# Performance work log

Hardware: AMD Instinct MI355X
Metric: run time of the kernel (lower is better)

The kernel has to match this reference:

```python
import jax, jax.numpy as jnp
import numpy as np

GROUPS = 64; SIDE = 8; STEPS = 8
TAU = 1.0; FLOOR = 1e-4; EPS = 1e-4
MU = 1.0; DT = 0.1; GAMMA = 0.1
FLOW_W = 1.0; LOCAL_W = 0.5; KEEP_RATIO = 0.5


def _with_floor(m):
    n = m.shape[-1]
    mask = 1.0 - jnp.eye(n, dtype=m.dtype)
    return jnp.maximum(m * mask, FLOOR * mask)


def _norm_scores(s):
    mean = s.mean(axis=1, keepdims=True)
    std = jnp.clip(s.std(axis=1, ddof=1, keepdims=True), 1e-6, None)  # torch unbiased std
    return (s - mean) / std


def _router_core(tokens, cls_token, W, grid_h, grid_w):
    B, P, D = tokens.shape
    # group ids from patch grid position (patch_indices defaults to arange)
    pi = jnp.broadcast_to(jnp.arange(P), (B, P))
    row, col = pi // grid_w, pi % grid_w
    gh = -(-grid_h // SIDE); gw = -(-grid_w // SIDE)  # ceil div
    gid = jnp.minimum(row // gh, SIDE - 1) * SIDE + jnp.minimum(col // gw, SIDE - 1)  # [B,P]
    # mean-pool tokens per group (scatter_add + count)
    seg = jax.vmap(lambda t, g: jax.ops.segment_sum(t, g, num_segments=GROUPS))
    grouped = seg(tokens, gid)                                 # [B,G,D]
    counts = seg(jnp.ones((B, P, 1), tokens.dtype), gid)       # [B,G,1]
    grouped = grouped / jnp.maximum(counts, 1.0)
    nodes = jnp.concatenate([cls_token[:, None, :], grouped], axis=1)  # [B,G+1,D]
    # pairwise conductance: project, l2-normalize, squared cdist, exp kernel
    proj = jnp.einsum('bnd,ed->bne', nodes, W)  # Linear (no bias): x @ W.T
    proj = proj / jnp.maximum(jnp.linalg.norm(proj, axis=-1, keepdims=True), 1e-12)
    sq = jnp.sum(proj * proj, axis=-1)
    d2 = jnp.maximum(sq[:, :, None] + sq[:, None, :]
                     - 2.0 * jnp.einsum('bnd,bmd->bnm', proj, proj), 0.0)
    C = _with_floor(jnp.exp(-d2 / TAU))
    C = 0.5 * (C + jnp.swapaxes(C, -1, -2))  # symmetric
    # source: cls node injects, groups drain
    source = jnp.full((B, GROUPS + 1), -1.0 / GROUPS, C.dtype).at[:, 0].set(1.0)
    N = GROUPS + 1
    I = jnp.eye(N, dtype=C.dtype)
    d_list, q_list = [C], []
    for _ in range(STEPS):
        deg = C.sum(-1)
        system = deg[:, :, None] * I - C + EPS * I            # Laplacian + eps*I
        p = jnp.linalg.solve(system, source[..., None])[..., 0]
        flow = C * (p[:, :, None] - p[:, None, :])
        q_list.append(flow)
        r = jnp.abs(flow) ** MU
        r = r / (1.0 + r)
        C = C + DT * (r - GAMMA * C)
        C = _with_floor(jnp.maximum(C, 0.0))
        C = _with_floor(0.5 * (C + jnp.swapaxes(C, -1, -2)))
        d_list.append(C)
    return C, jnp.stack(d_list, 1), jnp.stack(q_list, 1), gid


def setup_inputs() -> dict:
    key = jax.random.key(0)
    k1, k2, k3, k4 = jax.random.split(key, 4)
    B, P, D = 64, 576, 768
    return {
        'tokens': jax.random.normal(k1, (B, P, D), jnp.float32),
        'cls_token': jax.random.normal(k2, (B, D), jnp.float32),
        'W': jax.random.normal(k3, (D, D), jnp.float32) / np.sqrt(D),
        'local_scores': jax.random.normal(k4, (B, P), jnp.float32),
        'grid_h': 24,
        'grid_w': 24,
    }


def reference(tokens, cls_token, W, local_scores, grid_h, grid_w):
    B, P, _ = tokens.shape
    final_d, d_hist, q_hist, gid = _router_core(tokens, cls_token, W, grid_h, grid_w)
    routing = final_d[:, 1:, 1:]
    routing = routing / jnp.clip(routing.sum(-1, keepdims=True), 1e-6, None)
    group_flow = jnp.abs(q_hist[:, -1, 1:, :]).sum(-1)        # [B,G]
    group_scores = jnp.take_along_axis(_norm_scores(group_flow), gid, axis=1)
    token_scores = FLOW_W * group_scores + LOCAL_W * _norm_scores(local_scores)
    keep_count = max(1, int(round(P * KEEP_RATIO)))
    _, topk = jax.lax.top_k(token_scores, keep_count)
    patch_keep_mask = jnp.zeros((B, P), bool).at[jnp.arange(B)[:, None], topk].set(True)
    keep_mask = jnp.concatenate([jnp.ones((B, 1), bool), patch_keep_mask], axis=1)
    delta = d_hist[:, 1:] - d_hist[:, :-1]
    aux_sparse = final_d[:, 1:, 1:].sum(axis=(-1, -2)).mean()
    aux_stable = jnp.abs(delta).sum(axis=(-1, -2, -3)).mean()
    return (keep_mask, patch_keep_mask, gid, group_scores, d_hist, q_hist,
            routing, aux_sparse, aux_stable)
```

## Files before the change

kernel.cpp:

```cpp
#include <hip/hip_runtime.h>
#include <stdint.h>

#define NB 64
#define NP 576
#define ND 768
#define NG 64
#define NN 65
#define NSTEPS 8
#define FLOORV 1.0e-4f
#define EPSV   1.0e-4f
#define DTV    0.1f
#define GAMMAV 0.1f
#define KEEPC  288
#define PITCH  67

__global__ __launch_bounds__(256) void k_group_means(const float* __restrict__ tokens,
                                                     const float* __restrict__ cls,
                                                     float* __restrict__ nodes,
                                                     const int* __restrict__ ghp,
                                                     const int* __restrict__ gwp) {
    int bx = blockIdx.x;
    int b = bx / NN, n = bx - b * NN;
    int tid = threadIdx.x;
    float* orow = nodes + (size_t)bx * ND;
    if (n == 0) {
        for (int d = tid; d < ND; d += 256) orow[d] = cls[(size_t)b * ND + d];
        return;
    }
    int grid_h = *ghp, grid_w = *gwp;
    int gh = (grid_h + 7) / 8, gw = (grid_w + 7) / 8;
    int g = n - 1, gr = g >> 3, gc = g & 7;
    int r0 = gr * gh, r1 = (gr == 7) ? grid_h : min((gr + 1) * gh, grid_h);
    int c0 = gc * gw, c1 = (gc == 7) ? grid_w : min((gc + 1) * gw, grid_w);
    int cnt = (r1 > r0 && c1 > c0) ? (r1 - r0) * (c1 - c0) : 0;
    float cf = (float)max(cnt, 1);
    const float* tb = tokens + (size_t)b * NP * ND;
    for (int d = tid; d < ND; d += 256) {
        float acc = 0.f;
        for (int r = r0; r < r1; ++r)
            for (int c = c0; c < c1; ++c)
                acc += tb[(size_t)(r * grid_w + c) * ND + d];
        orow[d] = acc / cf;
    }
}

__global__ __launch_bounds__(256) void k_gemm_nt(const float* __restrict__ A,
                                                 const float* __restrict__ Bm,
                                                 float* __restrict__ Cm) {
    __shared__ float As[32][68];
    __shared__ float Bs[32][68];
    int tid = threadIdx.x;
    int m0 = blockIdx.x * 64, n0 = blockIdx.y * 64;
    int tx = tid & 15, ty = tid >> 4;
    float acc[4][4];
#pragma unroll
    for (int i = 0; i < 4; ++i)
#pragma unroll
        for (int j = 0; j < 4; ++j) acc[i][j] = 0.f;
    int lrow = tid >> 3, lq = tid & 7;
    for (int k0 = 0; k0 < ND; k0 += 32) {
#pragma unroll
        for (int l = 0; l < 2; ++l) {
            int row = lrow + l * 32;
            float4 va = *(const float4*)&A[(size_t)(m0 + row) * ND + k0 + lq * 4];
            As[lq * 4 + 0][row] = va.x; As[lq * 4 + 1][row] = va.y;
            As[lq * 4 + 2][row] = va.z; As[lq * 4 + 3][row] = va.w;
            float4 vb = *(const float4*)&Bm[(size_t)(n0 + row) * ND + k0 + lq * 4];
            Bs[lq * 4 + 0][row] = vb.x; Bs[lq * 4 + 1][row] = vb.y;
            Bs[lq * 4 + 2][row] = vb.z; Bs[lq * 4 + 3][row] = vb.w;
        }
        __syncthreads();
#pragma unroll
        for (int kk = 0; kk < 32; ++kk) {
            float4 a4 = *(const float4*)&As[kk][ty * 4];
            float4 b4 = *(const float4*)&Bs[kk][tx * 4];
            float av[4] = {a4.x, a4.y, a4.z, a4.w};
            float bv[4] = {b4.x, b4.y, b4.z, b4.w};
#pragma unroll
            for (int i = 0; i < 4; ++i)
#pragma unroll
                for (int j = 0; j < 4; ++j) acc[i][j] += av[i] * bv[j];
        }
        __syncthreads();
    }
#pragma unroll
    for (int i = 0; i < 4; ++i) {
        float4 o = make_float4(acc[i][0], acc[i][1], acc[i][2], acc[i][3]);
        *(float4*)&Cm[(size_t)(m0 + ty * 4 + i) * ND + n0 + tx * 4] = o;
    }
}

__global__ __launch_bounds__(256) void k_normalize(float* __restrict__ proj, float* __restrict__ sqv) {
    int r = blockIdx.x, tid = threadIdx.x;
    __shared__ double red[8];
    __shared__ float invs;
    float* row = proj + (size_t)r * ND;
    double s = 0.0;
    for (int d = tid; d < ND; d += 256) { double v = (double)row[d]; s += v * v; }
#pragma unroll
    for (int off = 32; off; off >>= 1) s += __shfl_down(s, off, 64);
    int wid = tid >> 6, lane = tid & 63;
    if (lane == 0) red[wid] = s;
    __syncthreads();
    if (tid == 0) invs = (float)(1.0 / fmax(sqrt(red[0] + red[1] + red[2] + red[3]), 1e-12));
    __syncthreads();
    float inv = invs;
    double s2 = 0.0;
    for (int d = tid; d < ND; d += 256) {
        float v = row[d] * inv; row[d] = v; s2 += (double)v * (double)v;
    }
#pragma unroll
    for (int off = 32; off; off >>= 1) s2 += __shfl_down(s2, off, 64);
    __syncthreads();
    if (lane == 0) red[wid] = s2;
    __syncthreads();
    if (tid == 0) sqv[r] = (float)(red[0] + red[1] + red[2] + red[3]);
}

__global__ __launch_bounds__(256) void k_pairwise(const float* __restrict__ proj,
                                                  const float* __restrict__ sqv,
                                                  float* __restrict__ dhist) {
    int b = blockIdx.x, tid = threadIdx.x;
    int tx = tid & 15, ty = tid >> 4;
    __shared__ float Ps[NN][65];
    float acc[5][5];
#pragma unroll
    for (int a = 0; a < 5; ++a)
#pragma unroll
        for (int c = 0; c < 5; ++c) acc[a][c] = 0.f;
    const float* Pb = proj + (size_t)b * NN * ND;
    for (int k0 = 0; k0 < ND; k0 += 64) {
        __syncthreads();
        for (int idx = tid; idx < NN * 64; idx += 256) {
            int i = idx >> 6, kk = idx & 63;
            Ps[i][kk] = Pb[(size_t)i * ND + k0 + kk];
        }
        __syncthreads();
        for (int kk = 0; kk < 64; ++kk) {
            float av[5], bv[5];
#pragma unroll
            for (int a = 0; a < 5; ++a) { int i = ty + 16 * a; av[a] = (i < NN) ? Ps[i][kk] : 0.f; }
#pragma unroll
            for (int c = 0; c < 5; ++c) { int j = tx + 16 * c; bv[c] = (j < NN) ? Ps[j][kk] : 0.f; }
#pragma unroll
            for (int a = 0; a < 5; ++a)
#pragma unroll
                for (int c = 0; c < 5; ++c) acc[a][c] += av[a] * bv[c];
        }
    }
#pragma unroll
    for (int a = 0; a < 5; ++a)
#pragma unroll
        for (int c = 0; c < 5; ++c) {
            int i = ty + 16 * a, j = tx + 16 * c;
            if (i < NN && j < NN) {
                float d2 = fmaxf(sqv[b * NN + i] + sqv[b * NN + j] - 2.0f * acc[a][c], 0.f);
                double cv = exp(-(double)d2);
                float cf = (i == j) ? 0.f : fmaxf((float)cv, FLOORV);
                dhist[(size_t)b * 9 * NN * NN + (size_t)i * NN + j] = cf;
            }
        }
}

__global__ __launch_bounds__(256) void k_dynamics(float* __restrict__ dhist,
                                                  float* __restrict__ qhist,
                                                  double* __restrict__ part) {
    int b = blockIdx.x, tid = threadIdx.x;
    __shared__ float Cs[NN * NN];
    __shared__ float Aug[NN * PITCH];
    __shared__ float pd[NN];
    __shared__ double redd[8];
    float* C0 = dhist + (size_t)b * 9 * NN * NN;
    for (int t = tid; t < NN * NN; t += 256) Cs[t] = C0[t];
    __syncthreads();

    int r = tid >> 2, q = tid & 3;
    const int my_i = r + 1;
    double stable = 0.0, sparse = 0.0;

#pragma unroll 1
    for (int step = 0; step < NSTEPS; ++step) {
        for (int t = tid; t < NN * NN; t += 256) {
            int i = t / NN, j = t - i * NN;
            if (i != j) Aug[i * PITCH + j] = -Cs[t];
        }
        if (tid < NN) {
            float s = 0.f;
            const float* cr = Cs + tid * NN;
#pragma unroll 1
            for (int j = 0; j < NN; ++j) s += cr[j];
            Aug[tid * PITCH + tid] = s + EPSV;
            Aug[tid * PITCH + NN] = (tid == 0) ? 1.0f : (-1.0f / NG);
        }
        __syncthreads();

#pragma unroll 1
        for (int k = 0; k < NN - 1; ++k) {
            if (my_i > k) {
                float invdk = 1.0f / Aug[k * PITCH + k];
                float f = Aug[my_i * PITCH + k] * invdk;
                const float* prow = Aug + k * PITCH;
                float* mrow = Aug + my_i * PITCH;
#pragma unroll 2
                for (int j = k + 1 + q; j <= NN; j += 4)
                    mrow[j] -= f * prow[j];
            }
            __syncthreads();
        }

        if (tid < 64) {
            int lane = tid;
            int i_own = lane + 1;
            const float* mrow = Aug + i_own * PITCH;
            float inv_own = 1.0f / mrow[i_own];
            float rhs = mrow[NN];
            float acc = 0.f, p_own = 0.f;
#pragma unroll 2
            for (int i = NN - 1; i >= 1; --i) {
                float t = (rhs - acc) * inv_own;
                float pi = __shfl(t, i - 1, 64);
                if (i_own == i) p_own = t;
                acc += ((lane < i - 1) ? mrow[i] : 0.f) * pi;
                if (lane == 0) pd[i] = pi;
            }
            float sp0 = Cs[i_own] * p_own;
#pragma unroll
            for (int off = 32; off; off >>= 1) sp0 += __shfl_down(sp0, off, 64);
            if (lane == 0) pd[0] = (1.0f + sp0) / Aug[0];
        }
        __syncthreads();

        float* qout = qhist + ((size_t)b * NSTEPS + step) * NN * NN;
        float* dout = dhist + ((size_t)b * 9 + step + 1) * NN * NN;
        for (int t = tid; t < NN * NN; t += 256) {
            int i = t / NN, j = t - i * NN;
            float c = Cs[t];
            float fl = c * (pd[i] - pd[j]);
            qout[t] = fl;
            float rr = fabsf(fl); rr = rr / (1.0f + rr);
            float cn = c + DTV * (rr - GAMMAV * c);
            float cnf = (i == j) ? 0.0f : fmaxf(cn, FLOORV);
            Cs[t] = cnf;
            dout[t] = cnf;
            stable += fabs((double)cnf - (double)c);
            if (step == NSTEPS - 1 && i > 0 && j > 0) sparse += (double)cnf;
        }
        __syncthreads();
    }

#pragma unroll
    for (int off = 32; off; off >>= 1) {
        stable += __shfl_down(stable, off, 64);
        sparse += __shfl_down(sparse, off, 64);
    }
    int wid = tid >> 6, lane = tid & 63;
    if (lane == 0) { redd[wid] = stable; redd[4 + wid] = sparse; }
    __syncthreads();
    if (tid == 0) {
        part[b]      = redd[4] + redd[5] + redd[6] + redd[7];
        part[NB + b] = redd[0] + redd[1] + redd[2] + redd[3];
    }
}

__global__ __launch_bounds__(256) void k_scores(const float* __restrict__ qhist,
                                                const float* __restrict__ local,
                                                const int* __restrict__ ghp,
                                                const int* __restrict__ gwp,
                                                float* __restrict__ keep,
                                                float* __restrict__ patch,
                                                float* __restrict__ gidout,
                                                float* __restrict__ gsout) {
    int b = blockIdx.x, tid = threadIdx.x;
    __shared__ double gf[NG];
    __shared__ double ts[NP];
    __shared__ double red[8];
    __shared__ double stats[2];
    if (tid < NG) {
        const float* qrow = qhist + ((size_t)b * NSTEPS + (NSTEPS - 1)) * NN * NN + (size_t)(tid + 1) * NN;
        double s = 0.0;
        for (int j = 0; j < NN; ++j) s += fabs((double)qrow[j]);
        gf[tid] = s;
    }
    __syncthreads();
    if (tid < 64) {
        double v = gf[tid];
        double s = v;
#pragma unroll
        for (int off = 32; off; off >>= 1) s += __shfl_down(s, off, 64);
        double mean = __shfl(s, 0, 64) / (double)NG;
        double d = v - mean, ss = d * d;
#pragma unroll
        for (int off = 32; off; off >>= 1) ss += __shfl_down(ss, off, 64);
        if (tid == 0) { stats[0] = mean; stats[1] = 1.0 / fmax(sqrt(ss / (NG - 1)), 1e-6); }
    }
    const float* lrow = local + (size_t)b * NP;
    double s1 = 0.0;
    for (int p = tid; p < NP; p += 256) s1 += (double)lrow[p];
#pragma unroll
    for (int off = 32; off; off >>= 1) s1 += __shfl_down(s1, off, 64);
    int wid = tid >> 6, lane = tid & 63;
    if (lane == 0) red[wid] = s1;
    __syncthreads();
    double lmean = (red[0] + red[1] + red[2] + red[3]) / (double)NP;
    double s2 = 0.0;
    for (int p = tid; p < NP; p += 256) { double d = (double)lrow[p] - lmean; s2 += d * d; }
#pragma unroll
    for (int off = 32; off; off >>= 1) s2 += __shfl_down(s2, off, 64);
    __syncthreads();
    if (lane == 0) red[wid] = s2;
    __syncthreads();
    double linv = 1.0 / fmax(sqrt((red[0] + red[1] + red[2] + red[3]) / (double)(NP - 1)), 1e-6);
    double gmean = stats[0], ginv = stats[1];
    int grid_h = *ghp, grid_w = *gwp;
    int gh = (grid_h + 7) / 8, gw = (grid_w + 7) / 8;
    for (int p = tid; p < NP; p += 256) {
        int row = p / grid_w, col = p - row * grid_w;
        int g = min(row / gh, 7) * 8 + min(col / gw, 7);
        double gsc = (gf[g] - gmean) * ginv;
        double lsc = ((double)lrow[p] - lmean) * linv;
        ts[p] = gsc + 0.5 * lsc;
        gidout[(size_t)b * NP + p] = (float)g;
        gsout[(size_t)b * NP + p]  = (float)gsc;
    }
    __syncthreads();
    for (int p = tid; p < NP; p += 256) {
        double sp = ts[p];
        int c = 0;
        for (int qq = 0; qq < NP; ++qq) {
            double v = ts[qq];
            c += (v > sp) || (v == sp && qq < p);
        }
        float kf = (c < KEEPC) ? 1.0f : 0.0f;
        patch[(size_t)b * NP + p] = kf;
        keep[(size_t)b * (NP + 1) + 1 + p] = kf;
    }
    if (tid == 0) keep[(size_t)b * (NP + 1)] = 1.0f;
}

__global__ void k_routing(const float* __restrict__ dhist, float* __restrict__ rout) {
    int b = blockIdx.x, tid = threadIdx.x;
    const float* Crow = dhist + ((size_t)b * 9 + 8) * NN * NN + (size_t)(tid + 1) * NN + 1;
    double s = 0.0;
    for (int j = 0; j < NG; ++j) s += (double)Crow[j];
    double inv = 1.0 / fmax(s, 1e-6);
    float* orow = rout + ((size_t)b * NG + tid) * NG;
    for (int j = 0; j < NG; ++j) orow[j] = (float)((double)Crow[j] * inv);
}

__global__ void k_aux(const double* __restrict__ part, float* __restrict__ osp, float* __restrict__ ost) {
    int tid = threadIdx.x;
    double sp = part[tid], st = part[NB + tid];
#pragma unroll
    for (int off = 32; off; off >>= 1) {
        sp += __shfl_down(sp, off, 64);
        st += __shfl_down(st, off, 64);
    }
    if (tid == 0) { *osp = (float)(sp / NB); *ost = (float)(st / NB); }
}

extern "C" void kernel_launch(void* const* d_in, const int* in_sizes, int n_in,
                              void* d_out, int out_size, void* d_ws, size_t ws_size,
                              hipStream_t stream) {
    const float* tokens = (const float*)d_in[0];
    const float* cls    = (const float*)d_in[1];
    const float* W      = (const float*)d_in[2];
    const float* local  = (const float*)d_in[3];
    const int* ghp = (const int*)d_in[4];
    const int* gwp = (const int*)d_in[5];

    float* out = (float*)d_out;
    float* o_keep  = out;
    float* o_patch = o_keep + (size_t)NB * (NP + 1);
    float* o_gid   = o_patch + (size_t)NB * NP;
    float* o_gs    = o_gid + (size_t)NB * NP;
    float* o_dh    = o_gs + (size_t)NB * NP;
    float* o_qh    = o_dh + (size_t)NB * 9 * NN * NN;
    float* o_rt    = o_qh + (size_t)NB * NSTEPS * NN * NN;
    float* o_sp    = o_rt + (size_t)NB * NG * NG;
    float* o_st    = o_sp + 1;

    float* nodes = (float*)d_ws;
    float* proj  = nodes + (size_t)NB * NN * ND;
    float* sqv   = proj + (size_t)NB * NN * ND;
    double* part = (double*)(((uintptr_t)(sqv + NB * NN) + 15) & ~(uintptr_t)15);

    k_group_means<<<NB * NN, 256, 0, stream>>>(tokens, cls, nodes, ghp, gwp);
    dim3 g2((NB * NN) / 64, ND / 64);
    k_gemm_nt<<<g2, 256, 0, stream>>>(nodes, W, proj);
    k_normalize<<<NB * NN, 256, 0, stream>>>(proj, sqv);
    k_pairwise<<<NB, 256, 0, stream>>>(proj, sqv, o_dh);
    k_dynamics<<<NB, 256, 0, stream>>>(o_dh, o_qh, part);
    k_scores<<<NB, 256, 0, stream>>>(o_qh, local, ghp, gwp, o_keep, o_patch, o_gid, o_gs);
    k_routing<<<NB, 64, 0, stream>>>(o_dh, o_rt);
    k_aux<<<1, 64, 0, stream>>>(part, o_sp, o_st);
}
```

Baseline: 843.1 us.

## Blocked two-pivot Gaussian elimination with float4 row updates in dynamics solve

The in-shared-memory Gaussian elimination now removes two pivot columns per pass, using a rank-2 update, which halves the number of barrier-separated elimination steps. The row pitch is padded to 68 so rows can be read and written as float4 vectors. A fix-up pass then clears the sub-diagonal entry left in each odd row. The cost of full-row updates that include already-eliminated columns, plus extra divisions, is traded for fewer __syncthreads and wider LDS accesses. The reordered elimination may slightly change floating-point rounding.

New measurement: 719.2 us. 14.7% less time.

```diff
diff --git a/kernel.cpp b/kernel.cpp
--- a/kernel.cpp
+++ b/kernel.cpp
@@ -12,7 +12,7 @@
 #define DTV    0.1f
 #define GAMMAV 0.1f
 #define KEEPC  288
-#define PITCH  67
+#define PITCH2 68
 
 __global__ __launch_bounds__(256) void k_group_means(const float* __restrict__ tokens,
                                                      const float* __restrict__ cls,
@@ -167,7 +167,7 @@
                                                   double* __restrict__ part) {
     int b = blockIdx.x, tid = threadIdx.x;
     __shared__ float Cs[NN * NN];
-    __shared__ float Aug[NN * PITCH];
+    __shared__ float Aug[NN * PITCH2];
     __shared__ float pd[NN];
     __shared__ double redd[8];
     float* C0 = dhist + (size_t)b * 9 * NN * NN;
@@ -176,51 +176,101 @@
 
     int r = tid >> 2, q = tid & 3;
     const int my_i = r + 1;
+    float* mrow = Aug + my_i * PITCH2;
     double stable = 0.0, sparse = 0.0;
 
 #pragma unroll 1
     for (int step = 0; step < NSTEPS; ++step) {
-        for (int t = tid; t < NN * NN; t += 256) {
-            int i = t / NN, j = t - i * NN;
-            if (i != j) Aug[i * PITCH + j] = -Cs[t];
+        for (int t = tid; t < NN * PITCH2; t += 256) {
+            int i = t / PITCH2, j = t - i * PITCH2;
+            if (j != i && j != NN)
+                Aug[t] = (j < NN) ? -Cs[i * NN + j] : 0.f;
         }
         if (tid < NN) {
             float s = 0.f;
             const float* cr = Cs + tid * NN;
+#pragma unroll 4
+            for (int j = 0; j < NN; ++j) s += cr[j];
+            Aug[tid * PITCH2 + tid] = s + EPSV;
+            Aug[tid * PITCH2 + NN] = (tid == 0) ? 1.0f : (-1.0f / NG);
+        }
+        __syncthreads();
+
 #pragma unroll 1
-            for (int j = 0; j < NN; ++j) s += cr[j];
-            Aug[tid * PITCH + tid] = s + EPSV;
-            Aug[tid * PITCH + NN] = (tid == 0) ? 1.0f : (-1.0f / NG);
-        }
-        __syncthreads();
-
-#pragma unroll 1
-        for (int k = 0; k < NN - 1; ++k) {
-            if (my_i > k) {
-                float invdk = 1.0f / Aug[k * PITCH + k];
-                float f = Aug[my_i * PITCH + k] * invdk;
-                const float* prow = Aug + k * PITCH;
-                float* mrow = Aug + my_i * PITCH;
-#pragma unroll 2
-                for (int j = k + 1 + q; j <= NN; j += 4)
-                    mrow[j] -= f * prow[j];
+        for (int k = 0; k < NN - 1; k += 2) {
+            if (my_i > k + 1) {
+                const float* P = Aug + k * PITCH2;
+                const float* Q = P + PITCH2;
+                float Pk = P[k], Pk1 = P[k + 1];
+                float Qk = Q[k], Qk1 = Q[k + 1];
+                float Aik = mrow[k], Aik1 = mrow[k + 1];
+                float invP = 1.0f / Pk;
+                float h = Qk * invP;
+                float Qd = Qk1 - h * Pk1;
+                float f = Aik * invP;
+                float g = (Aik1 - f * Pk1) / Qd;
+                float c1 = f - g * h, c2 = g;
+                const float4* P4 = (const float4*)P;
+                const float4* Q4 = (const float4*)Q;
+                float4* M4 = (float4*)mrow;
+#pragma unroll
+                for (int u = 0; u < 4; ++u) {
+                    int t = q + 4 * u;
+                    float4 p = P4[t], qv = Q4[t], m = M4[t];
+                    m.x -= c1 * p.x + c2 * qv.x;
+                    m.y -= c1 * p.y + c2 * qv.y;
+                    m.z -= c1 * p.z + c2 * qv.z;
+                    m.w -= c1 * p.w + c2 * qv.w;
+                    M4[t] = m;
+                }
+                if (q == 0) {
+                    float4 p = P4[16], qv = Q4[16], m = M4[16];
+                    m.x -= c1 * p.x + c2 * qv.x;
+                    m.y -= c1 * p.y + c2 * qv.y;
+                    m.z -= c1 * p.z + c2 * qv.z;
+                    m.w -= c1 * p.w + c2 * qv.w;
+                    M4[16] = m;
+                }
             }
             __syncthreads();
         }
+
+        {
+            int fr = 2 * (tid >> 3) + 1;
+            int l8 = tid & 7;
+            float* R = Aug + fr * PITCH2;
+            const float* Pp = R - PITCH2;
+            float h = R[fr - 1] / Pp[fr - 1];
+            float4* R4 = (float4*)R;
+            const float4* Pp4 = (const float4*)Pp;
+#pragma unroll
+            for (int u = 0; u < 2; ++u) {
+                int t = l8 + 8 * u;
+                float4 a = R4[t], p = Pp4[t];
+                a.x -= h * p.x; a.y -= h * p.y; a.z -= h * p.z; a.w -= h * p.w;
+                R4[t] = a;
+            }
+            if (l8 == 0) {
+                float4 a = R4[16], p = Pp4[16];
+                a.x -= h * p.x; a.y -= h * p.y; a.z -= h * p.z; a.w -= h * p.w;
+                R4[16] = a;
+            }
+        }
+        __syncthreads();
 
         if (tid < 64) {
             int lane = tid;
             int i_own = lane + 1;
-            const float* mrow = Aug + i_own * PITCH;
-            float inv_own = 1.0f / mrow[i_own];
-            float rhs = mrow[NN];
+            const float* brow = Aug + i_own * PITCH2;
+            float inv_own = 1.0f / brow[i_own];
+            float rhs = brow[NN];
             float acc = 0.f, p_own = 0.f;
 #pragma unroll 2
             for (int i = NN - 1; i >= 1; --i) {
                 float t = (rhs - acc) * inv_own;
                 float pi = __shfl(t, i - 1, 64);
                 if (i_own == i) p_own = t;
-                acc += ((lane < i - 1) ? mrow[i] : 0.f) * pi;
+                acc += ((lane < i - 1) ? brow[i] : 0.f) * pi;
                 if (lane == 0) pd[i] = pi;
             }
             float sp0 = Cs[i_own] * p_own;
```
